# Optimization experiments

Measured on AMD Instinct MI355X. Metric: run time of the kernel, lower is better.

The kernel has to match this reference:

```python
import jax, jax.numpy as jnp
import numpy as np


def _position_table(seq_len, d_model, dtype):
    # position[i, j] = sin(i / 10000**((j+1)/d))  if j even
    #                  cos(i / 10000**((j+1)/d))  if j odd
    # (note the nonstandard (j+1)/d exponent, faithful to the source)
    i = jnp.arange(seq_len, dtype=dtype)[:, None]          # [S, 1]
    j = jnp.arange(d_model, dtype=dtype)[None, :]          # [1, D]
    pf = i / jnp.power(jnp.asarray(10000.0, dtype), (j + 1.0) / d_model)  # [S, D]
    even = (jnp.arange(d_model) % 2 == 0)[None, :]
    return jnp.where(even, jnp.sin(pf), jnp.cos(pf))       # [S, D]


def setup_inputs() -> dict:
    key = jax.random.key(0)
    x = jax.random.normal(key, (4, 8192, 1024), dtype=jnp.float32)
    return {"x": x}


def reference(x) -> jnp.ndarray:
    B, S, D = x.shape
    pos = _position_table(S, D, x.dtype)
    return x + pos[None, :, :]
```

## Files before the change

kernel.cpp:

```cpp
#include <hip/hip_runtime.h>
#include <math.h>

#define PE_S 8192
#define PE_D 1024
#define PE_B 4

#define PE_BLOCKS 2048
#define PE_THREADS 256
#define PE_QTOTAL (PE_B * PE_S * PE_D / 4)
#define PE_NT (PE_BLOCKS * PE_THREADS)
#define PE_ITERS (PE_QTOTAL / PE_NT)

typedef float f32x4 __attribute__((ext_vector_type(4)));

__device__ __forceinline__ float pe_sin(float fs, float wrev) {
    float t = fs * wrev;
    float r = t - floorf(t);
    r += fmaf(fs, wrev, -t);
    return __builtin_amdgcn_sinf(r);
}
__device__ __forceinline__ float pe_cos(float fs, float wrev) {
    float t = fs * wrev;
    float r = t - floorf(t);
    r += fmaf(fs, wrev, -t);
    return __builtin_amdgcn_cosf(r);
}

__global__ __launch_bounds__(PE_THREADS) void position_encoder_kernel(
    const float* __restrict__ x, float* __restrict__ out) {
    const int tid0 = blockIdx.x * blockDim.x + threadIdx.x;
    const int d0   = (tid0 & (PE_D / 4 - 1)) << 2;

    const float A2 = -0.012976281620653760f;
    const float C  = -2.6514961294723187f;
    const float w0 = exp2f(fmaf((float)(d0 + 1), A2, C));
    const float w1 = exp2f(fmaf((float)(d0 + 2), A2, C));
    const float w2 = exp2f(fmaf((float)(d0 + 3), A2, C));
    const float w3 = exp2f(fmaf((float)(d0 + 4), A2, C));

    f32x4 cur0 = *reinterpret_cast<const f32x4*>(x + (size_t)(tid0 + 0 * PE_NT) * 4);
    f32x4 cur1 = *reinterpret_cast<const f32x4*>(x + (size_t)(tid0 + 1 * PE_NT) * 4);

#pragma unroll
    for (int it = 0; it < PE_ITERS; ++it) {
        f32x4 nxt = {0.f, 0.f, 0.f, 0.f};
        if (it + 2 < PE_ITERS) {
            nxt = *reinterpret_cast<const f32x4*>(
                x + (size_t)(tid0 + (it + 2) * PE_NT) * 4);
        }

        const int q = tid0 + it * PE_NT;
        const int s = (q >> 8) & (PE_S - 1);
        const float fs = (float)s;

        f32x4 p;
        p.x = pe_sin(fs, w0);
        p.y = pe_cos(fs, w1);
        p.z = pe_sin(fs, w2);
        p.w = pe_cos(fs, w3);

        *reinterpret_cast<f32x4*>(out + (size_t)q * 4) = cur0 + p;

        cur0 = cur1;
        cur1 = nxt;
    }
}

extern "C" void kernel_launch(void* const* d_in, const int* in_sizes, int n_in,
                              void* d_out, int out_size, void* d_ws, size_t ws_size,
                              hipStream_t stream) {
    const float* x = (const float*)d_in[0];
    float* out = (float*)d_out;
    position_encoder_kernel<<<PE_BLOCKS, PE_THREADS, 0, stream>>>(x, out);
}
```

Before: 232.6 us.

## Batch all loads upfront per thread with fewer iterations and more blocks

Each thread now handles 8 float4 elements instead of 64. It issues all 8 global loads before any compute, separated by a scheduling barrier, and the grid grows to cover the tensor. This raises memory-level parallelism beyond the 2-deep software prefetch and is meant to hide load latency better. In exchange, the per-thread frequency setup (exp2 calls) is amortized over fewer elements, and register use per thread rises.

```diff
diff --git a/kernel.cpp b/kernel.cpp
--- a/kernel.cpp
+++ b/kernel.cpp
@@ -5,11 +5,11 @@
 #define PE_D 1024
 #define PE_B 4
 
-#define PE_BLOCKS 2048
+#define PE_K 8
+#define PE_QTOTAL (PE_B * PE_S * PE_D / 4)
+#define PE_NT (PE_QTOTAL / PE_K)
 #define PE_THREADS 256
-#define PE_QTOTAL (PE_B * PE_S * PE_D / 4)
-#define PE_NT (PE_BLOCKS * PE_THREADS)
-#define PE_ITERS (PE_QTOTAL / PE_NT)
+#define PE_BLOCKS (PE_NT / PE_THREADS)
 
 typedef float f32x4 __attribute__((ext_vector_type(4)));
 
@@ -28,8 +28,8 @@
 
 __global__ __launch_bounds__(PE_THREADS) void position_encoder_kernel(
     const float* __restrict__ x, float* __restrict__ out) {
-    const int tid0 = blockIdx.x * blockDim.x + threadIdx.x;
-    const int d0   = (tid0 & (PE_D / 4 - 1)) << 2;
+    const int tid = blockIdx.x * blockDim.x + threadIdx.x;
+    const int d0  = (tid & (PE_D / 4 - 1)) << 2;
 
     const float A2 = -0.012976281620653760f;
     const float C  = -2.6514961294723187f;
@@ -38,18 +38,18 @@
     const float w2 = exp2f(fmaf((float)(d0 + 3), A2, C));
     const float w3 = exp2f(fmaf((float)(d0 + 4), A2, C));
 
-    f32x4 cur0 = *reinterpret_cast<const f32x4*>(x + (size_t)(tid0 + 0 * PE_NT) * 4);
-    f32x4 cur1 = *reinterpret_cast<const f32x4*>(x + (size_t)(tid0 + 1 * PE_NT) * 4);
+    f32x4 v[PE_K];
+#pragma unroll
+    for (int k = 0; k < PE_K; ++k) {
+        v[k] = *reinterpret_cast<const f32x4*>(
+            x + (size_t)(tid + k * PE_NT) * 4);
+    }
+
+    __builtin_amdgcn_sched_barrier(0);
 
 #pragma unroll
-    for (int it = 0; it < PE_ITERS; ++it) {
-        f32x4 nxt = {0.f, 0.f, 0.f, 0.f};
-        if (it + 2 < PE_ITERS) {
-            nxt = *reinterpret_cast<const f32x4*>(
-                x + (size_t)(tid0 + (it + 2) * PE_NT) * 4);
-        }
-
-        const int q = tid0 + it * PE_NT;
+    for (int k = 0; k < PE_K; ++k) {
+        const int q = tid + k * PE_NT;
         const int s = (q >> 8) & (PE_S - 1);
         const float fs = (float)s;
 
@@ -59,10 +59,7 @@
         p.z = pe_sin(fs, w2);
         p.w = pe_cos(fs, w3);
 
-        *reinterpret_cast<f32x4*>(out + (size_t)q * 4) = cur0 + p;
-
-        cur0 = cur1;
-        cur1 = nxt;
+        *reinterpret_cast<f32x4*>(out + (size_t)q * 4) = v[k] + p;
     }
 }
 
```

Measured after the change: 241.6 us. +3.9%, slower.
